# Kernel optimization log

Hardware: AMD Instinct MI355X
Metric: run time of the kernel (lower is better)

The kernel has to match this reference:

```python
import jax, jax.numpy as jnp
import numpy as np

N, E, G = 50000, 1000000, 128          # nodes, edges, graphs
NODE_DIM, EDGE_DIM, HID, EMB = 8, 3, 32, 64


def setup_inputs() -> dict:
    key = jax.random.key(0)
    ks = list(jax.random.split(key, 16))
    def nrm(k, shape, s=1.0):
        return jax.random.normal(k, shape, dtype=jnp.float32) * s
    return {
        "x": nrm(ks[0], (N, NODE_DIM)),
        "edge_attr": nrm(ks[1], (E, EDGE_DIM)),
        "the_ratios": jax.random.uniform(ks[2], (5,), dtype=jnp.float32),
        "edge_index": jax.random.randint(ks[3], (2, E), 0, N),
        "batch": jnp.sort(jax.random.randint(ks[4], (N,), 0, G)),
        "the_ids": jax.random.randint(ks[5], (5,), 0, 118),
        # edge_nn: Linear(3,32) -> ReLU -> Linear(32, 8*32)
        "W1": nrm(ks[6], (EDGE_DIM, 32), 0.3), "b1": jnp.zeros((32,), jnp.float32),
        "W2": nrm(ks[7], (32, NODE_DIM * HID), 0.1), "b2": jnp.zeros((NODE_DIM * HID,), jnp.float32),
        "emb": nrm(ks[8], (118, EMB), 0.1),
        # NNConv root weight + bias
        "root": nrm(ks[9], (NODE_DIM, HID), 0.3), "conv_bias": jnp.zeros((HID,), jnp.float32),
        "fc0_w": nrm(ks[10], (HID + EMB, 64), 0.1), "fc0_b": jnp.zeros((64,), jnp.float32),
        "fc1_w": nrm(ks[11], (64, 32), 0.1), "fc1_b": jnp.zeros((32,), jnp.float32),
        "fc2_w": nrm(ks[12], (32, 1), 0.1), "fc2_b": jnp.zeros((1,), jnp.float32),
    }


def reference(x, edge_attr, the_ratios, edge_index, batch, the_ids,
              W1, b1, W2, b2, emb, root, conv_bias,
              fc0_w, fc0_b, fc1_w, fc1_b, fc2_w, fc2_b):
    src, dst = edge_index[0], edge_index[1]
    # per-edge weight matrix from edge MLP: [E, NODE_DIM, HID]
    h = jax.nn.relu(edge_attr @ W1 + b1)
    We = (h @ W2 + b2).reshape(E, NODE_DIM, HID)
    # gather source node feats, per-edge matmul: [E, HID]
    msg = jnp.einsum('ei,eio->eo', x[src], We)
    # scatter-mean to target nodes
    s = jax.ops.segment_sum(msg, dst, num_segments=N)
    cnt = jax.ops.segment_sum(jnp.ones((E,), msg.dtype), dst, num_segments=N)
    agg = s / jnp.maximum(cnt, 1.0)[:, None]
    # NNConv root transform + bias, then ReLU
    h_node = jax.nn.relu(x @ root + agg + conv_bias)
    # global mean pool over graphs
    gs = jax.ops.segment_sum(h_node, batch, num_segments=G)
    gc = jax.ops.segment_sum(jnp.ones((N,), h_node.dtype), batch, num_segments=G)
    pooled = gs / jnp.maximum(gc, 1.0)[:, None]
    # weighted element embedding, broadcast to all graphs
    u = jnp.sum(emb[the_ids] * the_ratios[:, None], axis=0)
    z = jnp.concatenate([pooled, jnp.broadcast_to(u, (G, EMB))], axis=1)
    z = jax.nn.relu(z @ fc0_w + fc0_b)
    z = jax.nn.relu(z @ fc1_w + fc1_b)
    return z @ fc2_w + fc2_b
```

## Files before the change

### kernel.cpp

```cpp
#include <hip/hip_runtime.h>

#define NODE_DIM 8

typedef __attribute__((ext_vector_type(8))) short short8;
typedef __attribute__((ext_vector_type(4))) float f32x4;

#define DOT8(xv, WT) ((xv)[0]*(WT)[0] + (xv)[1]*(WT)[1] + (xv)[2]*(WT)[2] + (xv)[3]*(WT)[3] + \
                      (xv)[4]*(WT)[4] + (xv)[5]*(WT)[5] + (xv)[6]*(WT)[6] + (xv)[7]*(WT)[7])

static __device__ __forceinline__ unsigned cvt_pk_bf16(float a, float b) {
    unsigned r;
    asm("v_cvt_pk_bf16_f32 %0, %1, %2" : "=v"(r) : "v"(a), "v"(b));
    return r;
}

__global__ __launch_bounds__(256, 4)
void edge_kernel(const float* __restrict__ x,
                 const float* __restrict__ ea,
                 const int* __restrict__ eidx,
                 const float* __restrict__ W1, const float* __restrict__ b1,
                 const float* __restrict__ W2, const float* __restrict__ b2,
                 float* __restrict__ s, int* __restrict__ cnt,
                 int E)
{
    __shared__ __align__(16) short lds_b[18 * 64 * 8];

    const int t = threadIdx.x;

    for (int f = t; f < 18 * 64 * 8; f += 256) {
        const int j   = f & 7;
        const int ln  = (f >> 3) & 63;
        const int fid = f >> 9;
        const int kk  = fid >> 1, ot = fid & 1;
        const int qq  = ln >> 4, ol = ln & 15;
        float v;
        if (kk < 8) v = W2[(kk * 4 + qq) * 256 + j * 32 + ot * 16 + ol];
        else        v = (qq == 0) ? b2[j * 32 + ot * 16 + ol] : 0.f;
        unsigned uv = __float_as_uint(v);
        uv = (uv + 0x7fffu + ((uv >> 16) & 1u)) >> 16;
        lds_b[f] = (short)uv;
    }
    __syncthreads();

    const int lane = t & 63;
    const int e_l  = lane & 15;
    const int q    = lane >> 4;

    float w10[8], w11[8], w12[8], b1r[8];
#pragma unroll
    for (int t2 = 0; t2 < 8; ++t2) {
        const int k = 4 * t2 + q;
        w10[t2] = W1[k]; w11[t2] = W1[32 + k]; w12[t2] = W1[64 + k]; b1r[t2] = b1[k];
    }

    const int wave = blockIdx.x * 4 + (t >> 6);
    const int nwav = gridDim.x * 4;
    const int ngrp = (E + 15) / 16;

    for (int g0 = 2 * wave; g0 < ngrp; g0 += 2 * nwav) {
        const bool v1    = (g0 + 1) < ngrp;
        const int  base0 = g0 * 16;
        const int  base1 = (v1 ? g0 + 1 : g0) * 16;

        int ej0 = base0 + e_l; if (ej0 >= E) ej0 = E - 1;
        int ej1 = base1 + e_l; if (ej1 >= E) ej1 = E - 1;

        const int src0 = eidx[ej0];
        const int dst0 = eidx[E + ej0];
        const int src1 = eidx[ej1];
        const int dst1 = eidx[E + ej1];
        const float ea00 = ea[3 * ej0], ea01 = ea[3 * ej0 + 1], ea02 = ea[3 * ej0 + 2];
        const float ea10 = ea[3 * ej1], ea11 = ea[3 * ej1 + 1], ea12 = ea[3 * ej1 + 2];
        const float4 xa0 = *(const float4*)(x + (size_t)(unsigned)src0 * 8);
        const float4 xb0 = *(const float4*)(x + (size_t)(unsigned)src0 * 8 + 4);
        const float4 xa1 = *(const float4*)(x + (size_t)(unsigned)src1 * 8);
        const float4 xb1 = *(const float4*)(x + (size_t)(unsigned)src1 * 8 + 4);
        const float xr0[8] = {xa0.x, xa0.y, xa0.z, xa0.w, xb0.x, xb0.y, xb0.z, xb0.w};
        const float xr1[8] = {xa1.x, xa1.y, xa1.z, xa1.w, xb1.x, xb1.y, xb1.z, xb1.w};

        float h0[8], h1[8];
#pragma unroll
        for (int t2 = 0; t2 < 8; ++t2) {
            const float z0 = b1r[t2] + ea00 * w10[t2] + ea01 * w11[t2] + ea02 * w12[t2];
            const float z1 = b1r[t2] + ea10 * w10[t2] + ea11 * w11[t2] + ea12 * w12[t2];
            h0[t2] = z0 > 0.f ? z0 : 0.f;
            h1[t2] = z1 > 0.f ? z1 : 0.f;
        }

        f32x4 a00 = {0.f, 0.f, 0.f, 0.f};
        f32x4 a01 = {0.f, 0.f, 0.f, 0.f};
        f32x4 a10 = {0.f, 0.f, 0.f, 0.f};
        f32x4 a11 = {0.f, 0.f, 0.f, 0.f};

        {
            union { short8 v; unsigned u[4]; } id0, id1;
#pragma unroll
            for (int p = 0; p < 4; ++p) {
                id0.u[p] = cvt_pk_bf16(xr0[2 * p], xr0[2 * p + 1]);
                id1.u[p] = cvt_pk_bf16(xr1[2 * p], xr1[2 * p + 1]);
            }
            const short8 bf0 = *(const short8*)&lds_b[(16 * 64 + lane) * 8];
            const short8 bf1 = *(const short8*)&lds_b[(17 * 64 + lane) * 8];
            a00 = __builtin_amdgcn_mfma_f32_16x16x32_bf16(id0.v, bf0, a00, 0, 0, 0);
            a01 = __builtin_amdgcn_mfma_f32_16x16x32_bf16(id0.v, bf1, a01, 0, 0, 0);
            a10 = __builtin_amdgcn_mfma_f32_16x16x32_bf16(id1.v, bf0, a10, 0, 0, 0);
            a11 = __builtin_amdgcn_mfma_f32_16x16x32_bf16(id1.v, bf1, a11, 0, 0, 0);
        }

#pragma unroll
        for (int kk = 0; kk < 8; ++kk) {
            const short8 bf0 = *(const short8*)&lds_b[((kk * 2 + 0) * 64 + lane) * 8];
            const short8 bf1 = *(const short8*)&lds_b[((kk * 2 + 1) * 64 + lane) * 8];
            const float hk0 = h0[kk], hk1 = h1[kk];
            union { short8 v; unsigned u[4]; } af0, af1;
#pragma unroll
            for (int p = 0; p < 4; ++p) {
                af0.u[p] = cvt_pk_bf16(hk0 * xr0[2 * p], hk0 * xr0[2 * p + 1]);
                af1.u[p] = cvt_pk_bf16(hk1 * xr1[2 * p], hk1 * xr1[2 * p + 1]);
            }
            a00 = __builtin_amdgcn_mfma_f32_16x16x32_bf16(af0.v, bf0, a00, 0, 0, 0);
            a01 = __builtin_amdgcn_mfma_f32_16x16x32_bf16(af0.v, bf1, a01, 0, 0, 0);
            a10 = __builtin_amdgcn_mfma_f32_16x16x32_bf16(af1.v, bf0, a10, 0, 0, 0);
            a11 = __builtin_amdgcn_mfma_f32_16x16x32_bf16(af1.v, bf1, a11, 0, 0, 0);
        }

#pragma unroll
        for (int r = 0; r < 4; ++r) {
            const int m   = q * 4 + r;
            const int dr0 = __shfl(dst0, m, 16);
            const int dr1 = __shfl(dst1, m, 16);
            if (base0 + m < E) {
                atomicAdd(&s[(size_t)(unsigned)dr0 * 32 + e_l],      a00[r]);
                atomicAdd(&s[(size_t)(unsigned)dr0 * 32 + 16 + e_l], a01[r]);
            }
            if (v1 && base1 + m < E) {
                atomicAdd(&s[(size_t)(unsigned)dr1 * 32 + e_l],      a10[r]);
                atomicAdd(&s[(size_t)(unsigned)dr1 * 32 + 16 + e_l], a11[r]);
            }
        }
        if (lane < 16) {
            if (base0 + e_l < E)       atomicAdd(&cnt[dst0], 1);
            if (v1 && base1 + e_l < E) atomicAdd(&cnt[dst1], 1);
        }
    }
}

__global__ __launch_bounds__(256)
void node_pool_kernel(const float* __restrict__ s,
                      const int* __restrict__ cnt,
                      const float* __restrict__ x,
                      const float* __restrict__ root,
                      const float* __restrict__ conv_bias,
                      const int* __restrict__ batch,
                      float* __restrict__ gsum, int N)
{
    __shared__ float red[256];
    const int t    = threadIdx.x;
    const int o    = t & 31;
    const int slot = t >> 5;
    const int base = blockIdx.x * 8;
    const int n    = base + slot;

    float rootr[8];
#pragma unroll
    for (int i = 0; i < 8; ++i) rootr[i] = root[i * 32 + o];
    const float cb = conv_bias[o];

    float v = 0.f;
    int   b = 0;
    if (n < N) {
        b = batch[n];
        const int   c    = cnt[n];
        const float rinv = 1.f / (float)(c > 1 ? c : 1);
        const float* xp  = x + (size_t)n * 8;
        float xv[8];
#pragma unroll
        for (int i = 0; i < 8; ++i) xv[i] = xp[i];
        const float t2 = s[(size_t)n * 32 + o] * rinv + cb + DOT8(xv, rootr);
        v = t2 > 0.f ? t2 : 0.f;
    }

    const int nlast  = (base + 7 < N) ? base + 7 : N - 1;
    const int bfirst = batch[base];
    const int blast  = batch[nlast];

    if (bfirst == blast && base + 7 < N) {
        red[t] = v;
        __syncthreads();
        if (t < 32) {
            float p = 0.f;
#pragma unroll
            for (int c2 = 0; c2 < 8; ++c2) p += red[t + 32 * c2];
            atomicAdd(&gsum[bfirst * 32 + t], p);
        }
    } else {
        if (n < N) atomicAdd(&gsum[b * 32 + o], v);
    }
}

__global__ __launch_bounds__(128)
void mlp_kernel(const float* __restrict__ gsum,
                const int* __restrict__ batch,
                const float* __restrict__ ratios,
                const int* __restrict__ ids,
                const float* __restrict__ emb,
                const float* __restrict__ fc0w, const float* __restrict__ fc0b,
                const float* __restrict__ fc1w, const float* __restrict__ fc1b,
                const float* __restrict__ fc2w, const float* __restrict__ fc2b,
                float* __restrict__ out, int N)
{
    __shared__ float zs[96];
    __shared__ float z1[64];
    __shared__ float z2[32];
    __shared__ int seg[2];

    const int g = blockIdx.x;
    const int t = threadIdx.x;

    if (t < 2) {
        const int target = g + t;
        int lo = 0, hi = N;
        while (lo < hi) {
            const int mid = (lo + hi) >> 1;
            if (batch[mid] < target) lo = mid + 1; else hi = mid;
        }
        seg[t] = lo;
    }
    __syncthreads();

    float c = (float)(seg[1] - seg[0]);
    if (c < 1.f) c = 1.f;

    if (t < 32) zs[t] = gsum[g * 32 + t] / c;
    if (t >= 32 && t < 96) {
        const int j = t - 32;
        float u = 0.f;
#pragma unroll
        for (int r = 0; r < 5; ++r) u += ratios[r] * emb[(size_t)ids[r] * 64 + j];
        zs[32 + j] = u;
    }
    __syncthreads();

    if (t < 64) {
        float a = fc0b[t];
        for (int k = 0; k < 96; ++k) a += zs[k] * fc0w[k * 64 + t];
        z1[t] = a > 0.f ? a : 0.f;
    }
    __syncthreads();

    if (t < 32) {
        float a = fc1b[t];
        for (int k = 0; k < 64; ++k) a += z1[k] * fc1w[k * 32 + t];
        z2[t] = a > 0.f ? a : 0.f;
    }
    __syncthreads();

    if (t == 0) {
        float a = fc2b[0];
        for (int k = 0; k < 32; ++k) a += z2[k] * fc2w[k];
        out[g] = a;
    }
}

extern "C" void kernel_launch(void* const* d_in, const int* in_sizes, int n_in,
                              void* d_out, int out_size, void* d_ws, size_t ws_size,
                              hipStream_t stream)
{
    const float* x         = (const float*)d_in[0];
    const float* ea        = (const float*)d_in[1];
    const float* ratios    = (const float*)d_in[2];
    const int*   eidx      = (const int*)  d_in[3];
    const int*   batch     = (const int*)  d_in[4];
    const int*   ids       = (const int*)  d_in[5];
    const float* W1        = (const float*)d_in[6];
    const float* b1        = (const float*)d_in[7];
    const float* W2        = (const float*)d_in[8];
    const float* b2        = (const float*)d_in[9];
    const float* emb       = (const float*)d_in[10];
    const float* root      = (const float*)d_in[11];
    const float* conv_bias = (const float*)d_in[12];
    const float* fc0w      = (const float*)d_in[13];
    const float* fc0b      = (const float*)d_in[14];
    const float* fc1w      = (const float*)d_in[15];
    const float* fc1b      = (const float*)d_in[16];
    const float* fc2w      = (const float*)d_in[17];
    const float* fc2b      = (const float*)d_in[18];

    const int N = in_sizes[0] / NODE_DIM;
    const int E = in_sizes[1] / 3;
    const int G = out_size;

    float* s    = (float*)d_ws;
    int*   cnt  = (int*)((char*)d_ws + (size_t)N * 32 * 4);
    float* gsum = (float*)((char*)d_ws + (size_t)N * 32 * 4 + (size_t)N * 4);
    (void)hipMemsetAsync(d_ws, 0, (size_t)N * 32 * 4 + (size_t)N * 4 + (size_t)G * 32 * 4, stream);

    edge_kernel<<<2048, 256, 0, stream>>>(x, ea, eidx, W1, b1, W2, b2, s, cnt, E);
    node_pool_kernel<<<(N + 7) / 8, 256, 0, stream>>>(s, cnt, x, root, conv_bias,
                                                      batch, gsum, N);
    mlp_kernel<<<G, 128, 0, stream>>>(gsum, batch, ratios, ids, emb,
                                      fc0w, fc0b, fc1w, fc1b, fc2w, fc2b,
                                      (float*)d_out, N);
}
```

Measured before the change: 272.7 us.

## Sort edges by destination via counting sort and merge atomics in CSR order

Adds a histogram, three-step prefix scan and permutation pass that orders edges by destination node, then processes edges in that order so consecutive edges with the same destination are summed in registers before each atomicAdd. This is meant to cut the number of global float atomics on the scatter-sum. In exchange it adds five extra kernel launches, integer atomics for the histogram and cursor, a serial single-thread scan of block partials, and an indirect perm gather that makes x/edge_attr reads random. The histogram also replaces the per-edge count the old kernel produced.

```diff
diff --git a/kernel.cpp b/kernel.cpp
--- a/kernel.cpp
+++ b/kernel.cpp
@@ -14,14 +14,244 @@
     return r;
 }
 
+
+__global__ __launch_bounds__(256)
+void hist_kernel(const int* __restrict__ eidx, int* __restrict__ hist, int E)
+{
+    for (int e = blockIdx.x * 256 + threadIdx.x; e < E; e += gridDim.x * 256)
+        atomicAdd(&hist[eidx[E + e]], 1);
+}
+
+__global__ __launch_bounds__(256)
+void scan_a(const int* __restrict__ hist, int* __restrict__ tmp,
+            int* __restrict__ partial, int N)
+{
+    __shared__ int lds[256];
+    const int t    = threadIdx.x;
+    const int base = blockIdx.x * 1024 + t * 4;
+    int v0 = 0, v1 = 0, v2 = 0, v3 = 0;
+    if (base + 0 < N) v0 = hist[base + 0];
+    if (base + 1 < N) v1 = hist[base + 1];
+    if (base + 2 < N) v2 = hist[base + 2];
+    if (base + 3 < N) v3 = hist[base + 3];
+    const int local = v0 + v1 + v2 + v3;
+    lds[t] = local;
+    __syncthreads();
+    for (int off = 1; off < 256; off <<= 1) {
+        const int add = (t >= off) ? lds[t - off] : 0;
+        __syncthreads();
+        lds[t] += add;
+        __syncthreads();
+    }
+    int run = lds[t] - local;
+    if (base + 0 < N) tmp[base + 0] = run; run += v0;
+    if (base + 1 < N) tmp[base + 1] = run; run += v1;
+    if (base + 2 < N) tmp[base + 2] = run; run += v2;
+    if (base + 3 < N) tmp[base + 3] = run;
+    if (t == 255) partial[blockIdx.x] = lds[255];
+}
+
+__global__ void scan_b(int* __restrict__ partial, int nb)
+{
+    if (blockIdx.x == 0 && threadIdx.x == 0) {
+        int run = 0;
+        for (int i = 0; i < nb; ++i) { const int v = partial[i]; partial[i] = run; run += v; }
+    }
+}
+
+__global__ __launch_bounds__(256)
+void scan_c(const int* __restrict__ tmp, const int* __restrict__ partial,
+            int* __restrict__ cursor, int N)
+{
+    const int i = blockIdx.x * 256 + threadIdx.x;
+    if (i < N) cursor[i] = tmp[i] + partial[i >> 10];
+}
+
+__global__ __launch_bounds__(256)
+void perm_kernel(const int* __restrict__ eidx, int* __restrict__ cursor,
+                 int* __restrict__ perm, int E)
+{
+    for (int e = blockIdx.x * 256 + threadIdx.x; e < E; e += gridDim.x * 256) {
+        const int d   = eidx[E + e];
+        const int pos = atomicAdd(&cursor[d], 1);
+        perm[pos] = e;
+    }
+}
+
 __global__ __launch_bounds__(256, 4)
-void edge_kernel(const float* __restrict__ x,
-                 const float* __restrict__ ea,
-                 const int* __restrict__ eidx,
-                 const float* __restrict__ W1, const float* __restrict__ b1,
-                 const float* __restrict__ W2, const float* __restrict__ b2,
-                 float* __restrict__ s, int* __restrict__ cnt,
-                 int E)
+void edge_csr(const float* __restrict__ x,
+              const float* __restrict__ ea,
+              const int* __restrict__ eidx,
+              const int* __restrict__ perm,
+              const float* __restrict__ W1, const float* __restrict__ b1,
+              const float* __restrict__ W2, const float* __restrict__ b2,
+              float* __restrict__ s, int E)
+{
+    __shared__ __align__(16) short lds_b[18 * 64 * 8];
+
+    const int t = threadIdx.x;
+
+    for (int f = t; f < 18 * 64 * 8; f += 256) {
+        const int j   = f & 7;
+        const int ln  = (f >> 3) & 63;
+        const int fid = f >> 9;
+        const int kk  = fid >> 1, ot = fid & 1;
+        const int qq  = ln >> 4, ol = ln & 15;
+        float v;
+        if (kk < 8) v = W2[(kk * 4 + qq) * 256 + j * 32 + ot * 16 + ol];
+        else        v = (qq == 0) ? b2[j * 32 + ot * 16 + ol] : 0.f;
+        unsigned uv = __float_as_uint(v);
+        uv = (uv + 0x7fffu + ((uv >> 16) & 1u)) >> 16;
+        lds_b[f] = (short)uv;
+    }
+    __syncthreads();
+
+    const int lane = t & 63;
+    const int e_l  = lane & 15;
+    const int q    = lane >> 4;
+
+    float w10[8], w11[8], w12[8], b1r[8];
+#pragma unroll
+    for (int t2 = 0; t2 < 8; ++t2) {
+        const int k = 4 * t2 + q;
+        w10[t2] = W1[k]; w11[t2] = W1[32 + k]; w12[t2] = W1[64 + k]; b1r[t2] = b1[k];
+    }
+
+    const int wave = blockIdx.x * 4 + (t >> 6);
+    const int nwav = gridDim.x * 4;
+    const int ngrp = (E + 15) / 16;
+
+    for (int g0 = 2 * wave; g0 < ngrp; g0 += 2 * nwav) {
+        const bool v1    = (g0 + 1) < ngrp;
+        const int  base0 = g0 * 16;
+        const int  base1 = (v1 ? g0 + 1 : g0) * 16;
+
+        int pj0 = base0 + e_l; if (pj0 >= E) pj0 = E - 1;
+        int pj1 = base1 + e_l; if (pj1 >= E) pj1 = E - 1;
+        const int ej0 = perm[pj0];
+        const int ej1 = perm[pj1];
+
+        const int src0 = eidx[ej0];
+        const int dst0 = eidx[E + ej0];
+        const int src1 = eidx[ej1];
+        const int dst1 = eidx[E + ej1];
+        const float ea00 = ea[3 * ej0], ea01 = ea[3 * ej0 + 1], ea02 = ea[3 * ej0 + 2];
+        const float ea10 = ea[3 * ej1], ea11 = ea[3 * ej1 + 1], ea12 = ea[3 * ej1 + 2];
+        const float4 xa0 = *(const float4*)(x + (size_t)(unsigned)src0 * 8);
+        const float4 xb0 = *(const float4*)(x + (size_t)(unsigned)src0 * 8 + 4);
+        const float4 xa1 = *(const float4*)(x + (size_t)(unsigned)src1 * 8);
+        const float4 xb1 = *(const float4*)(x + (size_t)(unsigned)src1 * 8 + 4);
+        const float xr0[8] = {xa0.x, xa0.y, xa0.z, xa0.w, xb0.x, xb0.y, xb0.z, xb0.w};
+        const float xr1[8] = {xa1.x, xa1.y, xa1.z, xa1.w, xb1.x, xb1.y, xb1.z, xb1.w};
+
+        int drA[4], drB[4];
+#pragma unroll
+        for (int r = 0; r < 4; ++r) {
+            drA[r] = __shfl(dst0, q * 4 + r, 16);
+            drB[r] = __shfl(dst1, q * 4 + r, 16);
+        }
+
+        float h0[8], h1[8];
+#pragma unroll
+        for (int t2 = 0; t2 < 8; ++t2) {
+            const float z0 = b1r[t2] + ea00 * w10[t2] + ea01 * w11[t2] + ea02 * w12[t2];
+            const float z1 = b1r[t2] + ea10 * w10[t2] + ea11 * w11[t2] + ea12 * w12[t2];
+            h0[t2] = z0 > 0.f ? z0 : 0.f;
+            h1[t2] = z1 > 0.f ? z1 : 0.f;
+        }
+
+        f32x4 a00 = {0.f, 0.f, 0.f, 0.f};
+        f32x4 a01 = {0.f, 0.f, 0.f, 0.f};
+        f32x4 a10 = {0.f, 0.f, 0.f, 0.f};
+        f32x4 a11 = {0.f, 0.f, 0.f, 0.f};
+
+        {
+            union { short8 v; unsigned u[4]; } id0, id1;
+#pragma unroll
+            for (int p = 0; p < 4; ++p) {
+                id0.u[p] = cvt_pk_bf16(xr0[2 * p], xr0[2 * p + 1]);
+                id1.u[p] = cvt_pk_bf16(xr1[2 * p], xr1[2 * p + 1]);
+            }
+            const short8 bf0 = *(const short8*)&lds_b[(16 * 64 + lane) * 8];
+            const short8 bf1 = *(const short8*)&lds_b[(17 * 64 + lane) * 8];
+            a00 = __builtin_amdgcn_mfma_f32_16x16x32_bf16(id0.v, bf0, a00, 0, 0, 0);
+            a01 = __builtin_amdgcn_mfma_f32_16x16x32_bf16(id0.v, bf1, a01, 0, 0, 0);
+            a10 = __builtin_amdgcn_mfma_f32_16x16x32_bf16(id1.v, bf0, a10, 0, 0, 0);
+            a11 = __builtin_amdgcn_mfma_f32_16x16x32_bf16(id1.v, bf1, a11, 0, 0, 0);
+        }
+
+#pragma unroll
+        for (int kk = 0; kk < 8; ++kk) {
+            const short8 bf0 = *(const short8*)&lds_b[((kk * 2 + 0) * 64 + lane) * 8];
+            const short8 bf1 = *(const short8*)&lds_b[((kk * 2 + 1) * 64 + lane) * 8];
+            const float hk0 = h0[kk], hk1 = h1[kk];
+            union { short8 v; unsigned u[4]; } af0, af1;
+#pragma unroll
+            for (int p = 0; p < 4; ++p) {
+                af0.u[p] = cvt_pk_bf16(hk0 * xr0[2 * p], hk0 * xr0[2 * p + 1]);
+                af1.u[p] = cvt_pk_bf16(hk1 * xr1[2 * p], hk1 * xr1[2 * p + 1]);
+            }
+            a00 = __builtin_amdgcn_mfma_f32_16x16x32_bf16(af0.v, bf0, a00, 0, 0, 0);
+            a01 = __builtin_amdgcn_mfma_f32_16x16x32_bf16(af0.v, bf1, a01, 0, 0, 0);
+            a10 = __builtin_amdgcn_mfma_f32_16x16x32_bf16(af1.v, bf0, a10, 0, 0, 0);
+            a11 = __builtin_amdgcn_mfma_f32_16x16x32_bf16(af1.v, bf1, a11, 0, 0, 0);
+        }
+
+        {
+            float run0 = a00[0], run1 = a01[0];
+            int   pd   = drA[0];
+            bool  pv   = (base0 + q * 4 + 0) < E;
+#pragma unroll
+            for (int r = 1; r < 4; ++r) {
+                const bool v = (base0 + q * 4 + r) < E;
+                const int  d = drA[r];
+                if (v && pv && d == pd) { run0 += a00[r]; run1 += a01[r]; }
+                else {
+                    if (pv) {
+                        atomicAdd(&s[(size_t)(unsigned)pd * 32 + e_l],      run0);
+                        atomicAdd(&s[(size_t)(unsigned)pd * 32 + 16 + e_l], run1);
+                    }
+                    run0 = a00[r]; run1 = a01[r]; pd = d; pv = v;
+                }
+            }
+            if (pv) {
+                atomicAdd(&s[(size_t)(unsigned)pd * 32 + e_l],      run0);
+                atomicAdd(&s[(size_t)(unsigned)pd * 32 + 16 + e_l], run1);
+            }
+        }
+        {
+            float run0 = a10[0], run1 = a11[0];
+            int   pd   = drB[0];
+            bool  pv   = v1 && ((base1 + q * 4 + 0) < E);
+#pragma unroll
+            for (int r = 1; r < 4; ++r) {
+                const bool v = v1 && ((base1 + q * 4 + r) < E);
+                const int  d = drB[r];
+                if (v && pv && d == pd) { run0 += a10[r]; run1 += a11[r]; }
+                else {
+                    if (pv) {
+                        atomicAdd(&s[(size_t)(unsigned)pd * 32 + e_l],      run0);
+                        atomicAdd(&s[(size_t)(unsigned)pd * 32 + 16 + e_l], run1);
+                    }
+                    run0 = a10[r]; run1 = a11[r]; pd = d; pv = v;
+                }
+            }
+            if (pv) {
+                atomicAdd(&s[(size_t)(unsigned)pd * 32 + e_l],      run0);
+                atomicAdd(&s[(size_t)(unsigned)pd * 32 + 16 + e_l], run1);
+            }
+        }
+    }
+}
+
+__global__ __launch_bounds__(256, 4)
+void edge_flat(const float* __restrict__ x,
+               const float* __restrict__ ea,
+               const int* __restrict__ eidx,
+               const float* __restrict__ W1, const float* __restrict__ b1,
+               const float* __restrict__ W2, const float* __restrict__ b2,
+               float* __restrict__ s, int* __restrict__ cnt,
+               int E)
 {
     __shared__ __align__(16) short lds_b[18 * 64 * 8];
 
@@ -290,13 +520,32 @@
     const int E = in_sizes[1] / 3;
     const int G = out_size;
 
-    float* s    = (float*)d_ws;
-    int*   cnt  = (int*)((char*)d_ws + (size_t)N * 32 * 4);
-    float* gsum = (float*)((char*)d_ws + (size_t)N * 32 * 4 + (size_t)N * 4);
-    (void)hipMemsetAsync(d_ws, 0, (size_t)N * 32 * 4 + (size_t)N * 4 + (size_t)G * 32 * 4, stream);
-
-    edge_kernel<<<2048, 256, 0, stream>>>(x, ea, eidx, W1, b1, W2, b2, s, cnt, E);
-    node_pool_kernel<<<(N + 7) / 8, 256, 0, stream>>>(s, cnt, x, root, conv_bias,
+    char* p = (char*)d_ws;
+    float* s      = (float*)p;                 p += (size_t)N * 32 * 4;
+    int*   hist   = (int*)p;                   p += (size_t)N * 4;
+    float* gsum   = (float*)p;                 p += (size_t)G * 32 * 4;
+    const size_t memset_bytes = (size_t)(p - (char*)d_ws);
+    int*   tmp    = (int*)p;                   p += (size_t)N * 4;
+    int*   part   = (int*)p;                   p += 256 * 4;
+    int*   cursor = (int*)p;                   p += (size_t)N * 4;
+    int*   perm   = (int*)p;                   p += (size_t)E * 4;
+    const size_t needed = (size_t)(p - (char*)d_ws);
+
+    (void)hipMemsetAsync(d_ws, 0, memset_bytes, stream);
+
+    if (ws_size >= needed) {
+        const int nb = (N + 1023) / 1024;
+        hist_kernel<<<1024, 256, 0, stream>>>(eidx, hist, E);
+        scan_a<<<nb, 256, 0, stream>>>(hist, tmp, part, N);
+        scan_b<<<1, 64, 0, stream>>>(part, nb);
+        scan_c<<<(N + 255) / 256, 256, 0, stream>>>(tmp, part, cursor, N);
+        perm_kernel<<<1024, 256, 0, stream>>>(eidx, cursor, perm, E);
+        edge_csr<<<2048, 256, 0, stream>>>(x, ea, eidx, perm, W1, b1, W2, b2, s, E);
+    } else {
+        edge_flat<<<2048, 256, 0, stream>>>(x, ea, eidx, W1, b1, W2, b2, s, hist, E);
+    }
+
+    node_pool_kernel<<<(N + 7) / 8, 256, 0, stream>>>(s, hist, x, root, conv_bias,
                                                       batch, gsum, N);
     mlp_kernel<<<G, 128, 0, stream>>>(gsum, batch, ratios, ids, emb,
                                       fc0w, fc0b, fc1w, fc1b, fc2w, fc2b,
```

After: 380.5 us. 1.4x slower.

## Fuse memset, edge, node-pool and MLP into one cooperative persistent kernel

Applied to the files above, without the earlier changes.

Replaces the memset plus three kernel launches with a single cooperative kernel of 1024 blocks. It zeroes the workspace in-kernel, runs the edge, node-pool and MLP phases in sequence, and separates them with grid-wide syncs. The intent is to remove launch gaps and per-kernel ramp-up and tail costs. In exchange, the edge phase runs on 1024 blocks instead of 2048, the node phase becomes a grid-stride loop, and each grid sync adds its own cost. The old multi-kernel path stays as a fallback if the cooperative launch fails.

```diff
diff --git a/kernel.cpp b/kernel.cpp
--- a/kernel.cpp
+++ b/kernel.cpp
@@ -1,4 +1,7 @@
 #include <hip/hip_runtime.h>
+#include <hip/hip_cooperative_groups.h>
+
+namespace cg = cooperative_groups;
 
 #define NODE_DIM 8
 
@@ -14,19 +17,12 @@
     return r;
 }
 
-__global__ __launch_bounds__(256, 4)
-void edge_kernel(const float* __restrict__ x,
-                 const float* __restrict__ ea,
-                 const int* __restrict__ eidx,
-                 const float* __restrict__ W1, const float* __restrict__ b1,
-                 const float* __restrict__ W2, const float* __restrict__ b2,
-                 float* __restrict__ s, int* __restrict__ cnt,
-                 int E)
-{
-    __shared__ __align__(16) short lds_b[18 * 64 * 8];
-
+
+static __device__ __forceinline__ void stage_b_frags(short* lds_b,
+                                                     const float* __restrict__ W2,
+                                                     const float* __restrict__ b2)
+{
     const int t = threadIdx.x;
-
     for (int f = t; f < 18 * 64 * 8; f += 256) {
         const int j   = f & 7;
         const int ln  = (f >> 3) & 63;
@@ -40,8 +36,19 @@
         uv = (uv + 0x7fffu + ((uv >> 16) & 1u)) >> 16;
         lds_b[f] = (short)uv;
     }
-    __syncthreads();
-
+}
+
+static __device__ __forceinline__ void edge_compute(const short* lds_b,
+                                                    const float* __restrict__ x,
+                                                    const float* __restrict__ ea,
+                                                    const int* __restrict__ eidx,
+                                                    const float* __restrict__ W1,
+                                                    const float* __restrict__ b1,
+                                                    float* __restrict__ s,
+                                                    int* __restrict__ cnt,
+                                                    int E)
+{
+    const int t    = threadIdx.x;
     const int lane = t & 63;
     const int e_l  = lane & 15;
     const int q    = lane >> 4;
@@ -145,6 +152,182 @@
     }
 }
 
+static __device__ __forceinline__ void node_phase(float* red,
+                                                  const float* __restrict__ s,
+                                                  const int* __restrict__ cnt,
+                                                  const float* __restrict__ x,
+                                                  const float* __restrict__ root,
+                                                  const float* __restrict__ conv_bias,
+                                                  const int* __restrict__ batch,
+                                                  float* __restrict__ gsum, int N)
+{
+    const int t    = threadIdx.x;
+    const int o    = t & 31;
+    const int slot = t >> 5;
+
+    float rootr[8];
+#pragma unroll
+    for (int i = 0; i < 8; ++i) rootr[i] = root[i * 32 + o];
+    const float cb = conv_bias[o];
+
+    for (int base = blockIdx.x * 8; base < N; base += gridDim.x * 8) {
+        __syncthreads();
+        const int n = base + slot;
+
+        float v = 0.f;
+        int   b = 0;
+        if (n < N) {
+            b = batch[n];
+            const int   c    = cnt[n];
+            const float rinv = 1.f / (float)(c > 1 ? c : 1);
+            const float* xp  = x + (size_t)n * 8;
+            float xv[8];
+#pragma unroll
+            for (int i = 0; i < 8; ++i) xv[i] = xp[i];
+            const float t2 = s[(size_t)n * 32 + o] * rinv + cb + DOT8(xv, rootr);
+            v = t2 > 0.f ? t2 : 0.f;
+        }
+
+        const int nlast  = (base + 7 < N) ? base + 7 : N - 1;
+        const int bfirst = batch[base];
+        const int blast  = batch[nlast];
+
+        if (bfirst == blast && base + 7 < N) {
+            red[t] = v;
+            __syncthreads();
+            if (t < 32) {
+                float p = 0.f;
+#pragma unroll
+                for (int c2 = 0; c2 < 8; ++c2) p += red[t + 32 * c2];
+                atomicAdd(&gsum[bfirst * 32 + t], p);
+            }
+        } else {
+            if (n < N) atomicAdd(&gsum[b * 32 + o], v);
+        }
+    }
+}
+
+static __device__ __forceinline__ void mlp_phase(float* lds,
+                                                 const float* __restrict__ gsum,
+                                                 const int* __restrict__ batch,
+                                                 const float* __restrict__ ratios,
+                                                 const int* __restrict__ ids,
+                                                 const float* __restrict__ emb,
+                                                 const float* __restrict__ fc0w, const float* __restrict__ fc0b,
+                                                 const float* __restrict__ fc1w, const float* __restrict__ fc1b,
+                                                 const float* __restrict__ fc2w, const float* __restrict__ fc2b,
+                                                 float* __restrict__ out, int N, int G)
+{
+    if (blockIdx.x >= (unsigned)G) return;
+
+    float* zs = lds;
+    float* z1 = lds + 96;
+    float* z2 = lds + 160;
+    int*   seg = (int*)(lds + 192);
+
+    const int g = blockIdx.x;
+    const int t = threadIdx.x;
+
+    if (t < 2) {
+        const int target = g + t;
+        int lo = 0, hi = N;
+        while (lo < hi) {
+            const int mid = (lo + hi) >> 1;
+            if (batch[mid] < target) lo = mid + 1; else hi = mid;
+        }
+        seg[t] = lo;
+    }
+    __syncthreads();
+
+    float c = (float)(seg[1] - seg[0]);
+    if (c < 1.f) c = 1.f;
+
+    if (t < 32) zs[t] = gsum[g * 32 + t] / c;
+    if (t >= 32 && t < 96) {
+        const int j = t - 32;
+        float u = 0.f;
+#pragma unroll
+        for (int r = 0; r < 5; ++r) u += ratios[r] * emb[(size_t)ids[r] * 64 + j];
+        zs[32 + j] = u;
+    }
+    __syncthreads();
+
+    if (t < 64) {
+        float a = fc0b[t];
+        for (int k = 0; k < 96; ++k) a += zs[k] * fc0w[k * 64 + t];
+        z1[t] = a > 0.f ? a : 0.f;
+    }
+    __syncthreads();
+
+    if (t < 32) {
+        float a = fc1b[t];
+        for (int k = 0; k < 64; ++k) a += z1[k] * fc1w[k * 32 + t];
+        z2[t] = a > 0.f ? a : 0.f;
+    }
+    __syncthreads();
+
+    if (t == 0) {
+        float a = fc2b[0];
+        for (int k = 0; k < 32; ++k) a += z2[k] * fc2w[k];
+        out[g] = a;
+    }
+}
+
+__global__ __launch_bounds__(256, 4)
+void fused_kernel(const float* __restrict__ x,
+                  const float* __restrict__ ea,
+                  const float* __restrict__ ratios,
+                  const int* __restrict__ eidx,
+                  const int* __restrict__ batch,
+                  const int* __restrict__ ids,
+                  const float* __restrict__ W1, const float* __restrict__ b1,
+                  const float* __restrict__ W2, const float* __restrict__ b2,
+                  const float* __restrict__ emb,
+                  const float* __restrict__ root,
+                  const float* __restrict__ conv_bias,
+                  const float* __restrict__ fc0w, const float* __restrict__ fc0b,
+                  const float* __restrict__ fc1w, const float* __restrict__ fc1b,
+                  const float* __restrict__ fc2w, const float* __restrict__ fc2b,
+                  float* __restrict__ s, int* __restrict__ cnt,
+                  float* __restrict__ gsum, float* __restrict__ out,
+                  int N, int E, int G)
+{
+    __shared__ __align__(16) short lds_b[18 * 64 * 8];
+
+    stage_b_frags(lds_b, W2, b2);
+
+    {
+        int* zp = (int*)s;
+        const int ndw = N * 32 + N + G * 32;
+        for (int i = blockIdx.x * 256 + threadIdx.x; i < ndw; i += gridDim.x * 256)
+            zp[i] = 0;
+    }
+    cg::this_grid().sync();
+
+    edge_compute(lds_b, x, ea, eidx, W1, b1, s, cnt, E);
+    cg::this_grid().sync();
+
+    node_phase((float*)lds_b, s, cnt, x, root, conv_bias, batch, gsum, N);
+    cg::this_grid().sync();
+
+    mlp_phase((float*)lds_b, gsum, batch, ratios, ids, emb,
+              fc0w, fc0b, fc1w, fc1b, fc2w, fc2b, out, N, G);
+}
+
+__global__ __launch_bounds__(256, 4)
+void edge_kernel(const float* __restrict__ x,
+                 const float* __restrict__ ea,
+                 const int* __restrict__ eidx,
+                 const float* __restrict__ W1, const float* __restrict__ b1,
+                 const float* __restrict__ W2, const float* __restrict__ b2,
+                 float* __restrict__ s, int* __restrict__ cnt, int E)
+{
+    __shared__ __align__(16) short lds_b[18 * 64 * 8];
+    stage_b_frags(lds_b, W2, b2);
+    __syncthreads();
+    edge_compute(lds_b, x, ea, eidx, W1, b1, s, cnt, E);
+}
+
 __global__ __launch_bounds__(256)
 void node_pool_kernel(const float* __restrict__ s,
                       const int* __restrict__ cnt,
@@ -155,47 +338,7 @@
                       float* __restrict__ gsum, int N)
 {
     __shared__ float red[256];
-    const int t    = threadIdx.x;
-    const int o    = t & 31;
-    const int slot = t >> 5;
-    const int base = blockIdx.x * 8;
-    const int n    = base + slot;
-
-    float rootr[8];
-#pragma unroll
-    for (int i = 0; i < 8; ++i) rootr[i] = root[i * 32 + o];
-    const float cb = conv_bias[o];
-
-    float v = 0.f;
-    int   b = 0;
-    if (n < N) {
-        b = batch[n];
-        const int   c    = cnt[n];
-        const float rinv = 1.f / (float)(c > 1 ? c : 1);
-        const float* xp  = x + (size_t)n * 8;
-        float xv[8];
-#pragma unroll
-        for (int i = 0; i < 8; ++i) xv[i] = xp[i];
-        const float t2 = s[(size_t)n * 32 + o] * rinv + cb + DOT8(xv, rootr);
-        v = t2 > 0.f ? t2 : 0.f;
-    }
-
-    const int nlast  = (base + 7 < N) ? base + 7 : N - 1;
-    const int bfirst = batch[base];
-    const int blast  = batch[nlast];
-
-    if (bfirst == blast && base + 7 < N) {
-        red[t] = v;
-        __syncthreads();
-        if (t < 32) {
-            float p = 0.f;
-#pragma unroll
-            for (int c2 = 0; c2 < 8; ++c2) p += red[t + 32 * c2];
-            atomicAdd(&gsum[bfirst * 32 + t], p);
-        }
-    } else {
-        if (n < N) atomicAdd(&gsum[b * 32 + o], v);
-    }
+    node_phase(red, s, cnt, x, root, conv_bias, batch, gsum, N);
 }
 
 __global__ __launch_bounds__(128)
@@ -207,59 +350,11 @@
                 const float* __restrict__ fc0w, const float* __restrict__ fc0b,
                 const float* __restrict__ fc1w, const float* __restrict__ fc1b,
                 const float* __restrict__ fc2w, const float* __restrict__ fc2b,
-                float* __restrict__ out, int N)
-{
-    __shared__ float zs[96];
-    __shared__ float z1[64];
-    __shared__ float z2[32];
-    __shared__ int seg[2];
-
-    const int g = blockIdx.x;
-    const int t = threadIdx.x;
-
-    if (t < 2) {
-        const int target = g + t;
-        int lo = 0, hi = N;
-        while (lo < hi) {
-            const int mid = (lo + hi) >> 1;
-            if (batch[mid] < target) lo = mid + 1; else hi = mid;
-        }
-        seg[t] = lo;
-    }
-    __syncthreads();
-
-    float c = (float)(seg[1] - seg[0]);
-    if (c < 1.f) c = 1.f;
-
-    if (t < 32) zs[t] = gsum[g * 32 + t] / c;
-    if (t >= 32 && t < 96) {
-        const int j = t - 32;
-        float u = 0.f;
-#pragma unroll
-        for (int r = 0; r < 5; ++r) u += ratios[r] * emb[(size_t)ids[r] * 64 + j];
-        zs[32 + j] = u;
-    }
-    __syncthreads();
-
-    if (t < 64) {
-        float a = fc0b[t];
-        for (int k = 0; k < 96; ++k) a += zs[k] * fc0w[k * 64 + t];
-        z1[t] = a > 0.f ? a : 0.f;
-    }
-    __syncthreads();
-
-    if (t < 32) {
-        float a = fc1b[t];
-        for (int k = 0; k < 64; ++k) a += z1[k] * fc1w[k * 32 + t];
-        z2[t] = a > 0.f ? a : 0.f;
-    }
-    __syncthreads();
-
-    if (t == 0) {
-        float a = fc2b[0];
-        for (int k = 0; k < 32; ++k) a += z2[k] * fc2w[k];
-        out[g] = a;
-    }
+                float* __restrict__ out, int N, int G)
+{
+    __shared__ float lds[194];
+    mlp_phase(lds, gsum, batch, ratios, ids, emb,
+              fc0w, fc0b, fc1w, fc1b, fc2w, fc2b, out, N, G);
 }
 
 extern "C" void kernel_launch(void* const* d_in, const int* in_sizes, int n_in,
@@ -286,19 +381,37 @@
     const float* fc2w      = (const float*)d_in[17];
     const float* fc2b      = (const float*)d_in[18];
 
-    const int N = in_sizes[0] / NODE_DIM;
-    const int E = in_sizes[1] / 3;
-    const int G = out_size;
+    int N = in_sizes[0] / NODE_DIM;
+    int E = in_sizes[1] / 3;
+    int G = out_size;
 
     float* s    = (float*)d_ws;
     int*   cnt  = (int*)((char*)d_ws + (size_t)N * 32 * 4);
     float* gsum = (float*)((char*)d_ws + (size_t)N * 32 * 4 + (size_t)N * 4);
-    (void)hipMemsetAsync(d_ws, 0, (size_t)N * 32 * 4 + (size_t)N * 4 + (size_t)G * 32 * 4, stream);
-
+    float* outp = (float*)d_out;
+
+    void* kargs[] = {
+        (void*)&x, (void*)&ea, (void*)&ratios, (void*)&eidx, (void*)&batch,
+        (void*)&ids, (void*)&W1, (void*)&b1, (void*)&W2, (void*)&b2,
+        (void*)&emb, (void*)&root, (void*)&conv_bias,
+        (void*)&fc0w, (void*)&fc0b, (void*)&fc1w, (void*)&fc1b,
+        (void*)&fc2w, (void*)&fc2b,
+        (void*)&s, (void*)&cnt, (void*)&gsum, (void*)&outp,
+        (void*)&N, (void*)&E, (void*)&G
+    };
+    hipError_t err = hipLaunchCooperativeKernel((const void*)fused_kernel,
+                                                dim3(1024), dim3(256),
+                                                kargs, 0, stream);
+    if (err == hipSuccess) return;
+
+    (void)hipGetLastError();
+    (void)hipMemsetAsync(d_ws, 0,
+                         (size_t)N * 32 * 4 + (size_t)N * 4 + (size_t)G * 32 * 4,
+                         stream);
     edge_kernel<<<2048, 256, 0, stream>>>(x, ea, eidx, W1, b1, W2, b2, s, cnt, E);
     node_pool_kernel<<<(N + 7) / 8, 256, 0, stream>>>(s, cnt, x, root, conv_bias,
                                                       batch, gsum, N);
     mlp_kernel<<<G, 128, 0, stream>>>(gsum, batch, ratios, ids, emb,
                                       fc0w, fc0b, fc1w, fc1b, fc2w, fc2b,
-                                      (float*)d_out, N);
-}
+                                      outp, N, G);
+}
```

Result: slower. 559.3 us (+105.1%).

## Fuse node transform, graph pooling and MLP into one per-graph kernel

Applied to the files above, without the earlier changes.

Merges the node/pool kernel and the MLP head into a single kernel launched with one block per graph. Each block binary-searches its node segment in the sorted batch array, computes the node transform over that segment and reduces it in shared memory. This removes the gsum atomics, the gsum buffer from the memset, and one kernel launch. The trade-off is that only 128 blocks, each with 256 threads striding ~390 nodes, cover all 50k nodes, so parallelism is much lower than the previous 6250-block launch. The edge kernel is only split into helper functions with no behaviour change.

```diff
diff --git a/kernel.cpp b/kernel.cpp
--- a/kernel.cpp
+++ b/kernel.cpp
@@ -14,19 +14,12 @@
     return r;
 }
 
-__global__ __launch_bounds__(256, 4)
-void edge_kernel(const float* __restrict__ x,
-                 const float* __restrict__ ea,
-                 const int* __restrict__ eidx,
-                 const float* __restrict__ W1, const float* __restrict__ b1,
-                 const float* __restrict__ W2, const float* __restrict__ b2,
-                 float* __restrict__ s, int* __restrict__ cnt,
-                 int E)
-{
-    __shared__ __align__(16) short lds_b[18 * 64 * 8];
-
+
+static __device__ __forceinline__ void stage_b_frags(short* lds_b,
+                                                     const float* __restrict__ W2,
+                                                     const float* __restrict__ b2)
+{
     const int t = threadIdx.x;
-
     for (int f = t; f < 18 * 64 * 8; f += 256) {
         const int j   = f & 7;
         const int ln  = (f >> 3) & 63;
@@ -40,8 +33,19 @@
         uv = (uv + 0x7fffu + ((uv >> 16) & 1u)) >> 16;
         lds_b[f] = (short)uv;
     }
-    __syncthreads();
-
+}
+
+static __device__ __forceinline__ void edge_compute(const short* lds_b,
+                                                    const float* __restrict__ x,
+                                                    const float* __restrict__ ea,
+                                                    const int* __restrict__ eidx,
+                                                    const float* __restrict__ W1,
+                                                    const float* __restrict__ b1,
+                                                    float* __restrict__ s,
+                                                    int* __restrict__ cnt,
+                                                    int E)
+{
+    const int t    = threadIdx.x;
     const int lane = t & 63;
     const int e_l  = lane & 15;
     const int q    = lane >> 4;
@@ -145,77 +149,45 @@
     }
 }
 
+__global__ __launch_bounds__(256, 4)
+void edge_kernel(const float* __restrict__ x,
+                 const float* __restrict__ ea,
+                 const int* __restrict__ eidx,
+                 const float* __restrict__ W1, const float* __restrict__ b1,
+                 const float* __restrict__ W2, const float* __restrict__ b2,
+                 float* __restrict__ s, int* __restrict__ cnt, int E)
+{
+    __shared__ __align__(16) short lds_b[18 * 64 * 8];
+    stage_b_frags(lds_b, W2, b2);
+    __syncthreads();
+    edge_compute(lds_b, x, ea, eidx, W1, b1, s, cnt, E);
+}
+
 __global__ __launch_bounds__(256)
-void node_pool_kernel(const float* __restrict__ s,
-                      const int* __restrict__ cnt,
-                      const float* __restrict__ x,
-                      const float* __restrict__ root,
-                      const float* __restrict__ conv_bias,
-                      const int* __restrict__ batch,
-                      float* __restrict__ gsum, int N)
+void node_mlp_kernel(const float* __restrict__ s,
+                     const int* __restrict__ cnt,
+                     const float* __restrict__ x,
+                     const float* __restrict__ root,
+                     const float* __restrict__ conv_bias,
+                     const int* __restrict__ batch,
+                     const float* __restrict__ ratios,
+                     const int* __restrict__ ids,
+                     const float* __restrict__ emb,
+                     const float* __restrict__ fc0w, const float* __restrict__ fc0b,
+                     const float* __restrict__ fc1w, const float* __restrict__ fc1b,
+                     const float* __restrict__ fc2w, const float* __restrict__ fc2b,
+                     float* __restrict__ out, int N)
 {
     __shared__ float red[256];
+    __shared__ float zs[96];
+    __shared__ float z1[64];
+    __shared__ float z2[32];
+    __shared__ int   seg[2];
+
+    const int g    = blockIdx.x;
     const int t    = threadIdx.x;
     const int o    = t & 31;
     const int slot = t >> 5;
-    const int base = blockIdx.x * 8;
-    const int n    = base + slot;
-
-    float rootr[8];
-#pragma unroll
-    for (int i = 0; i < 8; ++i) rootr[i] = root[i * 32 + o];
-    const float cb = conv_bias[o];
-
-    float v = 0.f;
-    int   b = 0;
-    if (n < N) {
-        b = batch[n];
-        const int   c    = cnt[n];
-        const float rinv = 1.f / (float)(c > 1 ? c : 1);
-        const float* xp  = x + (size_t)n * 8;
-        float xv[8];
-#pragma unroll
-        for (int i = 0; i < 8; ++i) xv[i] = xp[i];
-        const float t2 = s[(size_t)n * 32 + o] * rinv + cb + DOT8(xv, rootr);
-        v = t2 > 0.f ? t2 : 0.f;
-    }
-
-    const int nlast  = (base + 7 < N) ? base + 7 : N - 1;
-    const int bfirst = batch[base];
-    const int blast  = batch[nlast];
-
-    if (bfirst == blast && base + 7 < N) {
-        red[t] = v;
-        __syncthreads();
-        if (t < 32) {
-            float p = 0.f;
-#pragma unroll
-            for (int c2 = 0; c2 < 8; ++c2) p += red[t + 32 * c2];
-            atomicAdd(&gsum[bfirst * 32 + t], p);
-        }
-    } else {
-        if (n < N) atomicAdd(&gsum[b * 32 + o], v);
-    }
-}
-
-__global__ __launch_bounds__(128)
-void mlp_kernel(const float* __restrict__ gsum,
-                const int* __restrict__ batch,
-                const float* __restrict__ ratios,
-                const int* __restrict__ ids,
-                const float* __restrict__ emb,
-                const float* __restrict__ fc0w, const float* __restrict__ fc0b,
-                const float* __restrict__ fc1w, const float* __restrict__ fc1b,
-                const float* __restrict__ fc2w, const float* __restrict__ fc2b,
-                float* __restrict__ out, int N)
-{
-    __shared__ float zs[96];
-    __shared__ float z1[64];
-    __shared__ float z2[32];
-    __shared__ int seg[2];
-
-    const int g = blockIdx.x;
-    const int t = threadIdx.x;
 
     if (t < 2) {
         const int target = g + t;
@@ -227,11 +199,35 @@
         seg[t] = lo;
     }
     __syncthreads();
-
-    float c = (float)(seg[1] - seg[0]);
-    if (c < 1.f) c = 1.f;
-
-    if (t < 32) zs[t] = gsum[g * 32 + t] / c;
+    const int s0 = seg[0], s1 = seg[1];
+
+    float rootr[8];
+#pragma unroll
+    for (int i = 0; i < 8; ++i) rootr[i] = root[i * 32 + o];
+    const float cb = conv_bias[o];
+
+    float acc = 0.f;
+    for (int n = s0 + slot; n < s1; n += 8) {
+        const int   c    = cnt[n];
+        const float rinv = 1.f / (float)(c > 1 ? c : 1);
+        const float* xp  = x + (size_t)n * 8;
+        float xv[8];
+#pragma unroll
+        for (int i = 0; i < 8; ++i) xv[i] = xp[i];
+        const float t2 = s[(size_t)n * 32 + o] * rinv + cb + DOT8(xv, rootr);
+        acc += t2 > 0.f ? t2 : 0.f;
+    }
+    red[t] = acc;
+    __syncthreads();
+
+    if (t < 32) {
+        float p = 0.f;
+#pragma unroll
+        for (int c2 = 0; c2 < 8; ++c2) p += red[t + 32 * c2];
+        float c = (float)(s1 - s0);
+        if (c < 1.f) c = 1.f;
+        zs[t] = p / c;
+    }
     if (t >= 32 && t < 96) {
         const int j = t - 32;
         float u = 0.f;
@@ -290,15 +286,14 @@
     const int E = in_sizes[1] / 3;
     const int G = out_size;
 
-    float* s    = (float*)d_ws;
-    int*   cnt  = (int*)((char*)d_ws + (size_t)N * 32 * 4);
-    float* gsum = (float*)((char*)d_ws + (size_t)N * 32 * 4 + (size_t)N * 4);
-    (void)hipMemsetAsync(d_ws, 0, (size_t)N * 32 * 4 + (size_t)N * 4 + (size_t)G * 32 * 4, stream);
+    float* s   = (float*)d_ws;
+    int*   cnt = (int*)((char*)d_ws + (size_t)N * 32 * 4);
+
+    (void)hipMemsetAsync(d_ws, 0, (size_t)N * 32 * 4 + (size_t)N * 4, stream);
 
     edge_kernel<<<2048, 256, 0, stream>>>(x, ea, eidx, W1, b1, W2, b2, s, cnt, E);
-    node_pool_kernel<<<(N + 7) / 8, 256, 0, stream>>>(s, cnt, x, root, conv_bias,
-                                                      batch, gsum, N);
-    mlp_kernel<<<G, 128, 0, stream>>>(gsum, batch, ratios, ids, emb,
-                                      fc0w, fc0b, fc1w, fc1b, fc2w, fc2b,
-                                      (float*)d_out, N);
-}
+    node_mlp_kernel<<<G, 256, 0, stream>>>(s, cnt, x, root, conv_bias, batch,
+                                           ratios, ids, emb,
+                                           fc0w, fc0b, fc1w, fc1b, fc2w, fc2b,
+                                           (float*)d_out, N);
+}
```

Result: slower. 278.2 us (+2.0%).
